# Performance work log

Measured on AMD Instinct MI355X. Metric: run time of the kernel, lower is better.

Reference implementation:

```python
import jax, jax.numpy as jnp
import numpy as np

EPS = 1e-8

def setup_inputs() -> dict:
    key = jax.random.key(0)
    ks = jax.random.split(key, 5)
    N, Cin, Cout, K, H, W = 16, 512, 512, 3, 64, 64
    return {
        "x": jax.random.normal(ks[0], (N, Cin, H, W), dtype=jnp.float32),
        "s": jax.random.normal(ks[1], (N, Cin), dtype=jnp.float32),
        "noise": jax.random.normal(ks[2], (N, Cout, H, W), dtype=jnp.float32),
        "w": jax.random.normal(ks[3], (Cout, Cin, K, K), dtype=jnp.float32),
        "b": jax.random.normal(ks[4], (Cout,), dtype=jnp.float32),
    }

def reference(x, s, noise, w, b):
    # Demodulation coefficient: d[n,o] = rsqrt(sum_{c,kh,kw} (w[o,c]*s[n,c])^2 + eps)
    # einsum: (s^2)[n,c] . (w^2 summed over kh,kw)[o,c] -> [n,o]
    w2 = jnp.sum(w * w, axis=(2, 3))                      # [Cout, Cin]
    d = jax.lax.rsqrt(jnp.einsum('nc,oc->no', s * s, w2) + EPS)  # [N, Cout]
    # Fold per-sample modulation into the input, demodulation into the output
    # (mathematically identical to grouped conv with per-sample modulated weights).
    x_mod = x * s[:, :, None, None]                       # [N, Cin, H, W]
    y = jax.lax.conv_general_dilated(
        x_mod, w,
        window_strides=(1, 1),
        padding='SAME',
        dimension_numbers=('NCHW', 'OIHW', 'NCHW'),
    )                                                     # [N, Cout, H, W]
    y = y * d[:, :, None, None] + b[None, :, None, None] + noise
    return jnp.where(y >= 0, y, 0.2 * y)  # LeakyReLU(0.2)
```

## Files before the change

kernel.cpp:

```cpp
#include <hip/hip_runtime.h>
#include <cstdint>
#include <cstddef>

typedef __attribute__((ext_vector_type(8))) short bf16x8;
typedef __attribute__((ext_vector_type(4))) float floatx4;

#define NBATCH 16
#define CIN    512
#define COUT   512
#define HH     64
#define WW     64
#define HP     66
#define XSLOT  72
#define XSZ    (4 * 66 * XSLOT)
#define ASZ    (128 * XSLOT)

static __device__ __forceinline__ unsigned short f2bf(float f) {
  union { float f; unsigned u; } cv; cv.f = f;
  unsigned u = cv.u;
  return (unsigned short)((u + 0x7FFFu + ((u >> 16) & 1u)) >> 16);
}

__global__ void k_wprep(const float* __restrict__ w, unsigned short* __restrict__ wr,
                        float* __restrict__ w2t) {
  int o = blockIdx.x;
  int c = blockIdx.y * 256 + threadIdx.x;
  const float* wp = w + ((size_t)o * CIN + c) * 9;
  float v[9]; float sum = 0.f;
#pragma unroll
  for (int r = 0; r < 9; ++r) { v[r] = wp[r]; sum += v[r] * v[r]; }
  w2t[(size_t)c * COUT + o] = sum;
#pragma unroll
  for (int r = 0; r < 9; ++r)
    wr[((size_t)r * COUT + o) * CIN + c] = f2bf(v[r]);
}

__global__ void k_dcoef(const float* __restrict__ s, const float* __restrict__ w2t,
                        float* __restrict__ d) {
  __shared__ float s2[CIN];
  int n = blockIdx.y;
  int o = blockIdx.x * 256 + threadIdx.x;
  for (int c = threadIdx.x; c < CIN; c += 256) {
    float sv = s[n * CIN + c]; s2[c] = sv * sv;
  }
  __syncthreads();
  float sum = 0.f;
  for (int c = 0; c < CIN; ++c) sum += s2[c] * w2t[(size_t)c * COUT + o];
  d[n * COUT + o] = rsqrtf(sum + 1e-8f);
}

__global__ void k_xmod(const float* __restrict__ x, const float* __restrict__ s,
                       unsigned short* __restrict__ xmp) {
  __shared__ __align__(16) unsigned short tile[WW * 520];
  int tid  = threadIdx.x;
  int n    = blockIdx.x >> 6;
  int h    = blockIdx.x & 63;
  int wcol = tid & 63;
  int grp  = tid >> 6;
#pragma unroll
  for (int i = 0; i < 16; ++i) {
    int c0 = (i * 4 + grp) * 8;
    bf16x8 pk;
#pragma unroll
    for (int j = 0; j < 8; ++j) {
      int c = c0 + j;
      float v = x[(((size_t)n * CIN + c) * HH + h) * WW + wcol] * s[n * CIN + c];
      pk[j] = (short)f2bf(v);
    }
    *(bf16x8*)(tile + wcol * 520 + c0) = pk;
  }
  __syncthreads();
#pragma unroll
  for (int i = 0; i < 16; ++i) {
    int wv = i * 4 + grp;
    bf16x8 v = *(const bf16x8*)(tile + wv * 520 + wcol * 8);
    *(bf16x8*)(xmp + (((size_t)n * HP + (h + 1)) * HP + (wv + 1)) * CIN + wcol * 8) = v;
  }
}

__global__ __launch_bounds__(256, 2)
void k_conv(const unsigned short* __restrict__ xmp, const unsigned short* __restrict__ wr,
            const float* __restrict__ d, const float* __restrict__ bias,
            const float* __restrict__ noise, float* __restrict__ out) {
  __shared__ __align__(16) unsigned short smem[XSZ + ASZ];
  unsigned short* Xs = smem;
  unsigned short* As = smem + XSZ;

  int tid  = threadIdx.x;
  int lane = tid & 63;
  int l15  = lane & 15;
  int quad = lane >> 4;
  int wv   = tid >> 6;
  int wrow = wv & 1;
  int woc  = wv >> 1;

  int bx  = blockIdx.x;
  int n   = bx >> 5;
  int h0  = (bx & 31) * 2;
  int ocb = blockIdx.y * 128;

  floatx4 acc[4][4];
#pragma unroll
  for (int a = 0; a < 4; ++a)
#pragma unroll
    for (int b = 0; b < 4; ++b)
#pragma unroll
      for (int q = 0; q < 4; ++q) acc[a][b][q] = 0.f;

  for (int cb = 0; cb < 8; ++cb) {
    int c0 = cb * 64;
    {
      bf16x8 xv[8];
#pragma unroll
      for (int i = 0; i < 8; ++i) {
        int idx = i * 256 + tid;
        int row = idx / 528;
        int rem = idx - row * 528;
        int col = rem >> 3, ch = rem & 7;
        xv[i] = *(const bf16x8*)(xmp + (((size_t)n * HP + (h0 + row)) * HP + col) * CIN + c0 + ch * 8);
      }
#pragma unroll
      for (int i = 0; i < 8; ++i) {
        int idx = i * 256 + tid;
        int row = idx / 528;
        int rem = idx - row * 528;
        int col = rem >> 3, ch = rem & 7;
        *(bf16x8*)(Xs + (row * 66 + col) * XSLOT + ch * 8) = xv[i];
      }
      if (tid < 64) {
        int rem = 464 + tid;
        int col = rem >> 3, ch = rem & 7;
        bf16x8 v = *(const bf16x8*)(xmp + (((size_t)n * HP + (h0 + 3)) * HP + col) * CIN + c0 + ch * 8);
        *(bf16x8*)(Xs + (3 * 66 + col) * XSLOT + ch * 8) = v;
      }
    }
#pragma unroll
    for (int i = 0; i < 4; ++i) {
      int idx = i * 256 + tid;
      int ol = idx >> 3, ch = idx & 7;
      bf16x8 v = *(const bf16x8*)(wr + ((size_t)(ocb + ol)) * CIN + c0 + ch * 8);
      *(bf16x8*)(As + ol * XSLOT + ch * 8) = v;
    }
    __syncthreads();

    for (int r = 0; r < 9; ++r) {
      bf16x8 wpre[4];
      if (r < 8) {
#pragma unroll
        for (int i = 0; i < 4; ++i) {
          int idx = i * 256 + tid;
          int ol = idx >> 3, ch = idx & 7;
          wpre[i] = *(const bf16x8*)(wr + ((size_t)((r + 1) * COUT) + ocb + ol) * CIN + c0 + ch * 8);
        }
      }
      int kh = r / 3;
      int kw = r - kh * 3;
      int xrow = wrow + kh;
#pragma unroll
      for (int ks = 0; ks < 2; ++ks) {
        bf16x8 af[4], bfv[4];
#pragma unroll
        for (int mf = 0; mf < 4; ++mf)
          af[mf] = *(const bf16x8*)(As + (woc * 64 + mf * 16 + l15) * XSLOT + ks * 32 + quad * 8);
#pragma unroll
        for (int nf = 0; nf < 4; ++nf)
          bfv[nf] = *(const bf16x8*)(Xs + (xrow * 66 + (nf * 16 + l15 + kw)) * XSLOT + ks * 32 + quad * 8);
#pragma unroll
        for (int mf = 0; mf < 4; ++mf)
#pragma unroll
          for (int nf = 0; nf < 4; ++nf)
            acc[mf][nf] = __builtin_amdgcn_mfma_f32_16x16x32_bf16(af[mf], bfv[nf], acc[mf][nf], 0, 0, 0);
      }
      __syncthreads();
      if (r < 8) {
#pragma unroll
        for (int i = 0; i < 4; ++i) {
          int idx = i * 256 + tid;
          int ol = idx >> 3, ch = idx & 7;
          *(bf16x8*)(As + ol * XSLOT + ch * 8) = wpre[i];
        }
        __syncthreads();
      }
    }
  }

  int h = h0 + wrow;
#pragma unroll
  for (int mf = 0; mf < 4; ++mf) {
#pragma unroll
    for (int i = 0; i < 4; ++i) {
      int o = ocb + woc * 64 + mf * 16 + quad * 4 + i;
      float dd = d[n * COUT + o];
      float bb = bias[o];
      size_t base = (((size_t)n * COUT + o) * HH + h) * WW;
#pragma unroll
      for (int nf = 0; nf < 4; ++nf) {
        int wc = nf * 16 + l15;
        float v = acc[mf][nf][i] * dd + bb + noise[base + wc];
        out[base + wc] = (v >= 0.f) ? v : 0.2f * v;
      }
    }
  }
}

extern "C" void kernel_launch(void* const* d_in, const int* in_sizes, int n_in,
                              void* d_out, int out_size, void* d_ws, size_t ws_size,
                              hipStream_t stream) {
  (void)in_sizes; (void)n_in; (void)out_size; (void)ws_size;
  const float* x     = (const float*)d_in[0];
  const float* s     = (const float*)d_in[1];
  const float* noise = (const float*)d_in[2];
  const float* w     = (const float*)d_in[3];
  const float* bias  = (const float*)d_in[4];
  float* out = (float*)d_out;

  char* ws = (char*)d_ws;
  const size_t XMP_BYTES = (size_t)NBATCH * HP * HP * CIN * 2;
  const size_t WR_BYTES  = (size_t)9 * COUT * CIN * 2;
  const size_t W2_BYTES  = (size_t)CIN * COUT * 4;
  unsigned short* xmp = (unsigned short*)ws;
  unsigned short* wrr = (unsigned short*)(ws + XMP_BYTES);
  float* w2t          = (float*)(ws + XMP_BYTES + WR_BYTES);
  float* dcoef        = (float*)(ws + XMP_BYTES + WR_BYTES + W2_BYTES);

  hipMemsetAsync(xmp, 0, XMP_BYTES, stream);
  k_wprep<<<dim3(COUT, 2),  256, 0, stream>>>(w, wrr, w2t);
  k_dcoef<<<dim3(2, NBATCH), 256, 0, stream>>>(s, w2t, dcoef);
  k_xmod <<<dim3(NBATCH * HH), 256, 0, stream>>>(x, s, xmp);
  k_conv <<<dim3(NBATCH * HH / 2, COUT / 128), 256, 0, stream>>>(xmp, wrr, dcoef, bias, noise, out);
}
```

Before: 684.8 us.

## Use async global-to-LDS loads with double-buffered weights, XOR swizzle, and halo-only zeroing

```diff
diff --git a/kernel.cpp b/kernel.cpp
--- a/kernel.cpp
+++ b/kernel.cpp
@@ -11,14 +11,33 @@
 #define HH     64
 #define WW     64
 #define HP     66
-#define XSLOT  72
-#define XSZ    (4 * 66 * XSLOT)
-#define ASZ    (128 * XSLOT)
+
+#define XCOLS  72
+#define XUS    (4 * XCOLS * 64)
+#define AUS    (128 * 64)
 
 static __device__ __forceinline__ unsigned short f2bf(float f) {
   union { float f; unsigned u; } cv; cv.f = f;
   unsigned u = cv.u;
   return (unsigned short)((u + 0x7FFFu + ((u >> 16) & 1u)) >> 16);
+}
+
+static __device__ __forceinline__ void async16(const unsigned short* g, unsigned short* l) {
+  __builtin_amdgcn_global_load_lds(
+      (const __attribute__((address_space(1))) void*)g,
+      (__attribute__((address_space(3))) void*)l, 16, 0, 0);
+}
+
+__global__ void k_zero(unsigned short* __restrict__ xmp) {
+  int slot = blockIdx.x;
+  int n    = blockIdx.y;
+  int h, w;
+  if (slot < 66)       { h = 0;              w = slot;       }
+  else if (slot < 132) { h = 65;             w = slot - 66;  }
+  else if (slot < 196) { h = slot - 132 + 1; w = 0;          }
+  else                 { h = slot - 196 + 1; w = 65;         }
+  unsigned* p = (unsigned*)(xmp + (((size_t)n * HP + h) * HP + w) * CIN);
+  p[threadIdx.x] = 0u;
 }
 
 __global__ void k_wprep(const float* __restrict__ w, unsigned short* __restrict__ wr,
@@ -82,22 +101,23 @@
 void k_conv(const unsigned short* __restrict__ xmp, const unsigned short* __restrict__ wr,
             const float* __restrict__ d, const float* __restrict__ bias,
             const float* __restrict__ noise, float* __restrict__ out) {
-  __shared__ __align__(16) unsigned short smem[XSZ + ASZ];
-  unsigned short* Xs = smem;
-  unsigned short* As = smem + XSZ;
-
-  int tid  = threadIdx.x;
-  int lane = tid & 63;
-  int l15  = lane & 15;
-  int quad = lane >> 4;
-  int wv   = tid >> 6;
-  int wrow = wv & 1;
-  int woc  = wv >> 1;
-
-  int bx  = blockIdx.x;
-  int n   = bx >> 5;
-  int h0  = (bx & 31) * 2;
-  int ocb = blockIdx.y * 128;
+  __shared__ __align__(16) unsigned short smem[XUS + 2 * AUS];
+  unsigned short* Xs  = smem;
+  unsigned short* As0 = smem + XUS;
+  unsigned short* As1 = smem + XUS + AUS;
+
+  const int tid  = threadIdx.x;
+  const int lane = tid & 63;
+  const int l15  = lane & 15;
+  const int quad = lane >> 4;
+  const int wv   = tid >> 6;
+  const int wrow = wv & 1;
+  const int woc  = wv >> 1;
+
+  const int bx  = blockIdx.x;
+  const int n   = bx >> 5;
+  const int h0  = (bx & 31) * 2;
+  const int ocb = blockIdx.y * 128;
 
   floatx4 acc[4][4];
 #pragma unroll
@@ -107,80 +127,79 @@
 #pragma unroll
       for (int q = 0; q < 4; ++q) acc[a][b][q] = 0.f;
 
+  auto stageX = [&](int cb) {
+    const int c0 = cb * 64;
+    const size_t grow = ((size_t)n * HP + (h0 + wv)) * HP;
+#pragma unroll
+    for (int t = 0; t < 9; ++t) {
+      int ci   = t * 64 + lane;
+      int col  = ci >> 3;
+      int ch   = ci & 7;
+      int colc = (col < 66) ? col : 65;
+      const unsigned short* g = xmp + (grow + colc) * CIN + c0 + ((ch ^ (col & 7)) << 3);
+      unsigned short* l = Xs + ((wv * 576 + t * 64) << 3);
+      async16(g, l);
+    }
+  };
+  auto stageW = [&](int r, int cb, unsigned short* buf) {
+    const int c0 = cb * 64;
+#pragma unroll
+    for (int t = 0; t < 4; ++t) {
+      int ci = wv * 256 + t * 64 + lane;
+      int ol = ci >> 3;
+      int ch = ci & 7;
+      const unsigned short* g =
+          wr + ((size_t)(r * COUT) + ocb + ol) * CIN + c0 + ((ch ^ (ol & 7)) << 3);
+      unsigned short* l = buf + ((wv * 256 + t * 64) << 3);
+      async16(g, l);
+    }
+  };
+
+  unsigned short* Asel[2] = {As0, As1};
+
+  stageX(0);
+  stageW(0, 0, As0);
+
   for (int cb = 0; cb < 8; ++cb) {
-    int c0 = cb * 64;
-    {
-      bf16x8 xv[8];
-#pragma unroll
-      for (int i = 0; i < 8; ++i) {
-        int idx = i * 256 + tid;
-        int row = idx / 528;
-        int rem = idx - row * 528;
-        int col = rem >> 3, ch = rem & 7;
-        xv[i] = *(const bf16x8*)(xmp + (((size_t)n * HP + (h0 + row)) * HP + col) * CIN + c0 + ch * 8);
+#pragma unroll
+    for (int r = 0; r < 9; ++r) {
+      if (r < 8) stageW(r + 1, cb, Asel[(r + 1) & 1]);
+      if (r < 8) asm volatile("s_waitcnt vmcnt(4)" ::: "memory");
+      else       asm volatile("s_waitcnt vmcnt(0)" ::: "memory");
+      __builtin_amdgcn_s_barrier();
+      asm volatile("" ::: "memory");
+
+      const unsigned short* Ab = Asel[r & 1];
+      const int kh = r / 3, kw = r - (r / 3) * 3;
+      const int xb = (wrow + kh) * XCOLS;
+      __builtin_amdgcn_s_setprio(1);
+#pragma unroll
+      for (int ks = 0; ks < 2; ++ks) {
+        bf16x8 af[4], bv[4];
+#pragma unroll
+        for (int mf = 0; mf < 4; ++mf) {
+          int cpos = ((ks << 2) | quad) ^ (l15 & 7);
+          af[mf] = *(const bf16x8*)(Ab + ((woc * 64 + mf * 16 + l15) << 6) + (cpos << 3));
+        }
+#pragma unroll
+        for (int nf = 0; nf < 4; ++nf) {
+          int slot = xb + nf * 16 + l15 + kw;
+          int cpos = ((ks << 2) | quad) ^ ((l15 + kw) & 7);
+          bv[nf] = *(const bf16x8*)(Xs + (slot << 6) + (cpos << 3));
+        }
+#pragma unroll
+        for (int mf = 0; mf < 4; ++mf)
+#pragma unroll
+          for (int nf = 0; nf < 4; ++nf)
+            acc[mf][nf] = __builtin_amdgcn_mfma_f32_16x16x32_bf16(af[mf], bv[nf], acc[mf][nf], 0, 0, 0);
       }
-#pragma unroll
-      for (int i = 0; i < 8; ++i) {
-        int idx = i * 256 + tid;
-        int row = idx / 528;
-        int rem = idx - row * 528;
-        int col = rem >> 3, ch = rem & 7;
-        *(bf16x8*)(Xs + (row * 66 + col) * XSLOT + ch * 8) = xv[i];
-      }
-      if (tid < 64) {
-        int rem = 464 + tid;
-        int col = rem >> 3, ch = rem & 7;
-        bf16x8 v = *(const bf16x8*)(xmp + (((size_t)n * HP + (h0 + 3)) * HP + col) * CIN + c0 + ch * 8);
-        *(bf16x8*)(Xs + (3 * 66 + col) * XSLOT + ch * 8) = v;
-      }
-    }
-#pragma unroll
-    for (int i = 0; i < 4; ++i) {
-      int idx = i * 256 + tid;
-      int ol = idx >> 3, ch = idx & 7;
-      bf16x8 v = *(const bf16x8*)(wr + ((size_t)(ocb + ol)) * CIN + c0 + ch * 8);
-      *(bf16x8*)(As + ol * XSLOT + ch * 8) = v;
-    }
-    __syncthreads();
-
-    for (int r = 0; r < 9; ++r) {
-      bf16x8 wpre[4];
-      if (r < 8) {
-#pragma unroll
-        for (int i = 0; i < 4; ++i) {
-          int idx = i * 256 + tid;
-          int ol = idx >> 3, ch = idx & 7;
-          wpre[i] = *(const bf16x8*)(wr + ((size_t)((r + 1) * COUT) + ocb + ol) * CIN + c0 + ch * 8);
-        }
-      }
-      int kh = r / 3;
-      int kw = r - kh * 3;
-      int xrow = wrow + kh;
-#pragma unroll
-      for (int ks = 0; ks < 2; ++ks) {
-        bf16x8 af[4], bfv[4];
-#pragma unroll
-        for (int mf = 0; mf < 4; ++mf)
-          af[mf] = *(const bf16x8*)(As + (woc * 64 + mf * 16 + l15) * XSLOT + ks * 32 + quad * 8);
-#pragma unroll
-        for (int nf = 0; nf < 4; ++nf)
-          bfv[nf] = *(const bf16x8*)(Xs + (xrow * 66 + (nf * 16 + l15 + kw)) * XSLOT + ks * 32 + quad * 8);
-#pragma unroll
-        for (int mf = 0; mf < 4; ++mf)
-#pragma unroll
-          for (int nf = 0; nf < 4; ++nf)
-            acc[mf][nf] = __builtin_amdgcn_mfma_f32_16x16x32_bf16(af[mf], bfv[nf], acc[mf][nf], 0, 0, 0);
-      }
-      __syncthreads();
-      if (r < 8) {
-#pragma unroll
-        for (int i = 0; i < 4; ++i) {
-          int idx = i * 256 + tid;
-          int ol = idx >> 3, ch = idx & 7;
-          *(bf16x8*)(As + ol * XSLOT + ch * 8) = wpre[i];
-        }
-        __syncthreads();
-      }
+      __builtin_amdgcn_s_setprio(0);
+      asm volatile("" ::: "memory");
+      __builtin_amdgcn_s_barrier();
+    }
+    if (cb < 7) {
+      stageX(cb + 1);
+      stageW(0, cb + 1, As0);
     }
   }
 
@@ -223,7 +242,7 @@
   float* w2t          = (float*)(ws + XMP_BYTES + WR_BYTES);
   float* dcoef        = (float*)(ws + XMP_BYTES + WR_BYTES + W2_BYTES);
 
-  hipMemsetAsync(xmp, 0, XMP_BYTES, stream);
+  k_zero <<<dim3(260, NBATCH), 256, 0, stream>>>(xmp);
   k_wprep<<<dim3(COUT, 2),  256, 0, stream>>>(w, wrr, w2t);
   k_dcoef<<<dim3(2, NBATCH), 256, 0, stream>>>(s, w2t, dcoef);
   k_xmod <<<dim3(NBATCH * HH), 256, 0, stream>>>(x, s, xmp);
```

After: 599.6 us. 12.4% less time.
